# Kernel tuning notes

Measured on AMD Instinct MI355X. Metric: run time of the kernel, lower is better.

The kernel has to match this reference:

```python
import jax, jax.numpy as jnp
import numpy as np

B, T, N = 8, 512, 64        # batch, seq_len, enc_in
E, H, P = 128, 256, 96      # embed_size, hidden_size, pred_len
LAMBDA = 0.001              # softshrink sparsity threshold
SCALE = 0.02


def _leaky(h):
    return jnp.where(h >= 0, h, 0.01 * h)


def _softshrink(y):
    return jnp.where(y > LAMBDA, y - LAMBDA, jnp.where(y < -LAMBDA, y + LAMBDA, jnp.zeros_like(y)))


def setup_inputs() -> dict:
    key = jax.random.key(0)
    ks = jax.random.split(key, 16)
    f32 = jnp.float32
    d = {
        "x": jax.random.normal(ks[0], (B, T, N), f32),
        "emb": jax.random.normal(ks[1], (1, E), f32),
        # MLP (embed_size -> hidden -> embed_size), stored as [in, out]
        "w1": SCALE * jax.random.normal(ks[2], (E, H), f32),
        "b1": SCALE * jax.random.normal(ks[3], (H,), f32),
        "w2": SCALE * jax.random.normal(ks[4], (H, E), f32),
        "b2": SCALE * jax.random.normal(ks[5], (E,), f32),
        # MLP_time (seq_len -> hidden -> seq_len)
        "tw1": SCALE * jax.random.normal(ks[6], (T, H), f32),
        "tb1": SCALE * jax.random.normal(ks[7], (H,), f32),
        "tw2": SCALE * jax.random.normal(ks[8], (H, T), f32),
        "tb2": SCALE * jax.random.normal(ks[9], (T,), f32),
        # fc (seq_len*embed -> hidden -> pred_len)
        "fw1": SCALE * jax.random.normal(ks[10], (T * E, H), f32),
        "fb1": SCALE * jax.random.normal(ks[11], (H,), f32),
        "fw2": SCALE * jax.random.normal(ks[12], (H, P), f32),
        "fb2": SCALE * jax.random.normal(ks[13], (P,), f32),
    }
    return d


def reference(x, emb, w1, b1, w2, b2, tw1, tb1, tw2, tb2, fw1, fb1, fw2, fb2):
    # x: [B, T, N]
    x_noD = jnp.transpose(x, (0, 2, 1))            # [B, N, T]
    xe = x_noD[..., None] * emb                    # tokenEmb -> [B, N, T, E]
    bias = xe + x_noD[..., None]

    # NorMLP_temporal: rfft over time, shared MLP on real/imag, softshrink, irfft
    xf = jnp.fft.rfft(xe, axis=2, norm="ortho")   # [B, N, T//2+1, E] complex64

    def mlp(z):
        return _leaky(z @ w1 + b1) @ w2 + b2

    yr = _softshrink(mlp(xf.real))
    yi = _softshrink(mlp(xf.imag))
    y = jax.lax.complex(yr, yi)
    xt = jnp.fft.irfft(y, n=T, axis=2, norm="ortho")  # [B, N, T, E]

    # NorMLP_temporal_WO_freq: MLP_time over last (time) dim of x_noD
    xn = _leaky(x_noD @ tw1 + tb1) @ tw2 + tb2        # [B, N, T]

    out = xt + xn[..., None] + bias                   # use_bias = 1

    flat = out.reshape(B, N, T * E)
    h = _leaky(flat @ fw1 + fb1) @ fw2 + fb2          # [B, N, P]
    return jnp.transpose(h, (0, 2, 1))                # [B, P, N]
```

## Files before the change

kernel.cpp:

```cpp
#include <hip/hip_runtime.h>
#include <hip/hip_bf16.h>


typedef unsigned int uint;
typedef unsigned short ushort_t;
typedef __attribute__((ext_vector_type(4))) float f32x4;
typedef __attribute__((ext_vector_type(8))) short short8;

#define LAMBDA_ 0.001f
#define RSQRT512 0.044194173824159220f

__device__ __forceinline__ ushort_t f2bf(float f) {
    uint u = __float_as_uint(f);
    uint r = (u + 0x7FFFu + ((u >> 16) & 1u)) >> 16;
    return (ushort_t)r;
}
__device__ __forceinline__ ushort_t f2bf_hw(float f) {
    union { __hip_bfloat16 h; ushort_t u; } c;
    c.h = __float2bfloat16(f);
    return c.u;
}
__device__ __forceinline__ float bf2f(ushort_t v) { return __uint_as_float(((uint)v) << 16); }
__device__ __forceinline__ float leaky_(float v) { return v >= 0.f ? v : 0.01f * v; }

__device__ __forceinline__ void gload_lds16(const ushort_t* g, ushort_t* l) {
    __builtin_amdgcn_global_load_lds((const __attribute__((address_space(1))) void*)g,
                                     (__attribute__((address_space(3))) void*)l, 16, 0, 0);
}

__device__ __forceinline__ void tile_loop512(const ushort_t* __restrict__ A, int lda,
                                             const ushort_t* __restrict__ Bm, int ldb,
                                             int m0, int n0, int k0, int kIters,
                                             f32x4 (&acc)[4][2],
                                             ushort_t (&As)[2][128 * 64], ushort_t (&Bs)[2][128 * 64],
                                             int tid, int lane, int wid, int wr, int wc) {
    int lrow = lane >> 3;
    int sg = (lane & 7) ^ lrow;
    auto issue = [&](int kt, int buf) {
        int kb = k0 + kt * 64;
        for (int i = 0; i < 2; ++i) {
            int rbase = wid * 16 + i * 8;
            gload_lds16(A + (size_t)(m0 + rbase + lrow) * lda + kb + sg * 8, &As[buf][wid * 1024 + i * 512]);
            gload_lds16(Bm + (size_t)(n0 + rbase + lrow) * ldb + kb + sg * 8, &Bs[buf][wid * 1024 + i * 512]);
        }
    };
    issue(0, 0);
    __syncthreads();
    int cur = 0;
    for (int kt = 0; kt < kIters; ++kt) {
        int nxt = cur ^ 1;
        if (kt + 1 < kIters) issue(kt + 1, nxt);
        __builtin_amdgcn_s_setprio(1);
        for (int ks = 0; ks < 2; ++ks) {
            short8 a[4], b[2];
            int sl = ks * 4 + (lane >> 4);
            for (int mi = 0; mi < 4; ++mi) {
                int row = wr * 64 + mi * 16 + (lane & 15);
                a[mi] = *(const short8*)&As[cur][row * 64 + ((sl ^ (row & 7)) << 3)];
            }
            for (int ni = 0; ni < 2; ++ni) {
                int row = wc * 32 + ni * 16 + (lane & 15);
                b[ni] = *(const short8*)&Bs[cur][row * 64 + ((sl ^ (row & 7)) << 3)];
            }
            for (int mi = 0; mi < 4; ++mi)
                for (int ni = 0; ni < 2; ++ni)
                    acc[mi][ni] = __builtin_amdgcn_mfma_f32_16x16x32_bf16(a[mi], b[ni], acc[mi][ni], 0, 0, 0);
        }
        __builtin_amdgcn_s_setprio(0);
        __syncthreads();
        cur = nxt;
    }
}

__global__ __launch_bounds__(256) void k_pre_plus(const float* __restrict__ x, const float* __restrict__ tw1,
                                                  const float* __restrict__ tw2, const float* __restrict__ fw1,
                                                  const float* __restrict__ emb, const float* __restrict__ w1,
                                                  const float* __restrict__ b1,
                                                  ushort_t* __restrict__ A1cat, ushort_t* __restrict__ B1cat,
                                                  ushort_t* __restrict__ Wt, ushort_t* __restrict__ tw2_bf,
                                                  ushort_t* __restrict__ fw1T,
                                                  float* __restrict__ u_g, int* __restrict__ idxs_g,
                                                  float* __restrict__ bpkey_g) {
    __shared__ float tile[64 * 65];
    __shared__ float key_s[256];
    __shared__ int idx_s[256];
    int bid = blockIdx.x;
    int tid = threadIdx.x;
    if (bid < 3072) {
        int region = bid >> 10;
        int id = ((bid & 1023) << 8) + tid;
        int a = id >> 9, c = id & 511;
        if (region == 0) {
            int f = (a <= 256) ? a : (a - 256);
            int m = (c * f) & 511;
            float ang = (float)m * (6.283185307179586f / 512.0f);
            float v = ((a <= 256) ? cosf(ang) : -sinf(ang)) * RSQRT512;
            ushort_t hi = f2bf(v);
            ushort_t lo = f2bf(v - bf2f(hi));
            size_t row = (size_t)a * 1536;
            B1cat[row + c] = hi;
            B1cat[row + 512 + c] = hi;
            B1cat[row + 1024 + c] = lo;
        } else if (region == 1) {
            int f = (a <= 256) ? a : (a - 256);
            int m = (c * f) & 511;
            float ang = (float)m * (6.283185307179586f / 512.0f);
            float v = ((a <= 256) ? cosf(ang) : -sinf(ang)) * RSQRT512;
            float sc = (a == 0 || a == 256) ? 1.0f : 2.0f;
            Wt[id] = f2bf(v * sc);
        } else {
            if ((bid & 1023) < 512) tw2_bf[id] = f2bf(tw2[id]);
        }
    } else if (bid < 3104) {
        int b = bid - 3072;
        int t0 = (b & 7) << 6, h0 = (b >> 3) << 6;
        float (*t64)[65] = (float(*)[65])tile;
        for (int i = 0; i < 16; ++i) {
            int idx = tid + i * 256;
            int r = idx >> 6, cc = idx & 63;
            t64[r][cc] = tw1[(size_t)(t0 + r) * 256 + h0 + cc];
        }
        __syncthreads();
        for (int i = 0; i < 16; ++i) {
            int idx = tid + i * 256;
            int rr = idx >> 6, cc2 = idx & 63;
            float v = t64[cc2][rr];
            ushort_t hi = f2bf(v);
            ushort_t lo = f2bf(v - bf2f(hi));
            size_t row = (size_t)(512 + h0 + rr) * 1536;
            int t = t0 + cc2;
            B1cat[row + t] = hi;
            B1cat[row + 512 + t] = hi;
            B1cat[row + 1024 + t] = lo;
        }
    } else if (bid < 3360) {
        int b = bid - 3104;
        int bb = b >> 5;
        int rem = b & 31;
        int t0 = (rem >> 1) << 5;
        int n0 = (rem & 1) << 5;
        int tx = tid & 31, ty = tid >> 5;
        float (*t32)[33] = (float(*)[33])tile;
        for (int i = 0; i < 4; ++i) {
            int tt = ty * 4 + i;
            t32[tt][tx] = x[(size_t)(bb * 512 + t0 + tt) * 64 + n0 + tx];
        }
        __syncthreads();
        for (int i = 0; i < 4; ++i) {
            int nn = ty * 4 + i;
            float v = t32[tx][nn];
            ushort_t hi = f2bf(v);
            ushort_t lo = f2bf(v - bf2f(hi));
            size_t row = (size_t)(bb * 64 + n0 + nn) * 1536;
            int t = t0 + tx;
            A1cat[row + t] = hi;
            A1cat[row + 512 + t] = lo;
            A1cat[row + 1024 + t] = hi;
        }
    } else if (bid < 7456) {
        int b = bid - 3360;
        int e  = b & 127;
        int hb = (b >> 7) & 3;
        int tt = b >> 9;
        int t0 = tt << 6, h0 = hb << 6;
        float (*t64)[65] = (float(*)[65])tile;
        for (int i = 0; i < 4; ++i) {
            int idx = tid + i * 256;
            int r = idx >> 4, c4 = idx & 15;
            const float* src = fw1 + ((size_t)(t0 + r) * 128 + e) * 256 + h0 + c4 * 4;
            float4 v = *(const float4*)src;
            t64[r][c4 * 4 + 0] = v.x;
            t64[r][c4 * 4 + 1] = v.y;
            t64[r][c4 * 4 + 2] = v.z;
            t64[r][c4 * 4 + 3] = v.w;
        }
        __syncthreads();
        for (int p = 0; p < 2; ++p) {
            int idx = tid + p * 256;
            int hh = idx >> 3, tg = idx & 7;
            short8 o;
            for (int j = 0; j < 8; ++j) o[j] = (short)f2bf(t64[tg * 8 + j][hh]);
            *(short8*)(fw1T + ((size_t)(h0 + hh) * 128 + e) * 512 + t0 + tg * 8) = o;
        }
    } else {
        float acc = 0.f;
#pragma unroll 8
        for (int e = 0; e < 128; ++e) acc += emb[e] * w1[e * 256 + tid];
        u_g[tid] = acc;
        float bb0 = b1[tid];
        key_s[tid] = (acc == 0.f) ? INFINITY : (-bb0 / acc);
        idx_s[tid] = tid;
        __syncthreads();
        for (int k = 2; k <= 256; k <<= 1) {
            for (int j = k >> 1; j > 0; j >>= 1) {
                int ixj = tid ^ j;
                if (ixj > tid) {
                    bool up = ((tid & k) == 0);
                    float a0 = key_s[tid], a1 = key_s[ixj];
                    if ((a0 > a1) == up) {
                        key_s[tid] = a1; key_s[ixj] = a0;
                        int t0 = idx_s[tid]; idx_s[tid] = idx_s[ixj]; idx_s[ixj] = t0;
                    }
                }
                __syncthreads();
            }
        }
        bpkey_g[tid] = key_s[tid];
        idxs_g[tid] = idx_s[tid];
    }
}

__global__ __launch_bounds__(256) void k_mid(const ushort_t* __restrict__ fw1T, const float* __restrict__ emb,
                                             const float* __restrict__ tb2,
                                             ushort_t* __restrict__ B1cat, ushort_t* __restrict__ F1sbf,
                                             float* __restrict__ p2v,
                                             const float* __restrict__ u_g, const float* __restrict__ b1,
                                             const float* __restrict__ w2, const float* __restrict__ b2,
                                             const int* __restrict__ idxs_g,
                                             ushort_t* __restrict__ Atab, ushort_t* __restrict__ Btab) {
    __shared__ float embs[128];
    __shared__ float red[256];
    __shared__ float sA[256], sB[256];
    int bid = blockIdx.x;
    int tid = threadIdx.x;
    if (bid < 256) {
        int h = bid;
        if (tid < 128) embs[tid] = 1.f + emb[tid];
        __syncthreads();
        int t2 = tid * 2;
        const ushort_t* base = fw1T + ((size_t)h << 16) + t2;
        float as0 = 0.f, as1 = 0.f, ae0 = 0.f, ae1 = 0.f;
#pragma unroll 4
        for (int e = 0; e < 128; ++e) {
            uint v = *(const uint*)(base + (size_t)e * 512);
            float v0 = bf2f((ushort_t)(v & 0xffff));
            float v1 = bf2f((ushort_t)(v >> 16));
            float w = embs[e];
            as0 += v0; as1 += v1;
            ae0 += w * v0; ae1 += w * v1;
        }
        *(uint*)(F1sbf + (size_t)h * 512 + t2) = (uint)f2bf(as0) | ((uint)f2bf(as1) << 16);
        ushort_t hi0 = f2bf(ae0), hi1 = f2bf(ae1);
        ushort_t lo0 = f2bf(ae0 - bf2f(hi0)), lo1 = f2bf(ae1 - bf2f(hi1));
        size_t row = (size_t)(768 + h) * 1536;
        uint hpk = (uint)hi0 | ((uint)hi1 << 16);
        *(uint*)(B1cat + row + t2) = hpk;
        *(uint*)(B1cat + row + 512 + t2) = hpk;
        *(uint*)(B1cat + row + 1024 + t2) = (uint)lo0 | ((uint)lo1 << 16);
        red[tid] = tb2[t2] * as0 + tb2[t2 + 1] * as1;
        __syncthreads();
        for (int off = 128; off > 0; off >>= 1) {
            if (tid < off) red[tid] += red[tid + off];
            __syncthreads();
        }
        if (tid == 0) p2v[h] = red[0];
    } else {
        int e = bid - 256, r = tid;
        float uu0 = u_g[r], bb0 = b1[r];
        float w0 = w2[r * 128 + e];
        float c = (uu0 < 0.f || (uu0 == 0.f && bb0 >= 0.f)) ? 1.0f : 0.01f;
        float bA = c * uu0 * w0, bB = c * bb0 * w0;
        int h = idxs_g[r];
        float uu = u_g[h], bb = b1[h];
        float w = w2[h * 128 + e];
        float sgn = (uu > 0.f) ? 0.99f : -0.99f;
        float dA = sgn * uu * w, dB = sgn * bb * w;
        sA[r] = bA; sB[r] = bB;
        __syncthreads();
        for (int off = 128; off > 0; off >>= 1) {
            if (r < off) { sA[r] += sA[r + off]; sB[r] += sB[r + off]; }
            __syncthreads();
        }
        float baseA = sA[0], baseB = sB[0] + b2[e];
        __syncthreads();
        sA[r] = dA; sB[r] = dB;
        __syncthreads();
        for (int off = 1; off < 256; off <<= 1) {
            float vA = (r >= off) ? sA[r - off] : 0.f;
            float vB = (r >= off) ? sB[r - off] : 0.f;
            __syncthreads();
            sA[r] += vA; sB[r] += vB;
            __syncthreads();
        }
        if (r == 0) { Atab[e] = f2bf(baseA); Btab[e] = f2bf(baseB); }
        Atab[(r + 1) * 128 + e] = f2bf(baseA + sA[r]);
        Btab[(r + 1) * 128 + e] = f2bf(baseB + sB[r]);
    }
}

__global__ __launch_bounds__(512) void k_big3(const ushort_t* __restrict__ Wt, const ushort_t* __restrict__ fw1T,
                                              ushort_t* __restrict__ M2T,
                                              const ushort_t* __restrict__ A1cat, const ushort_t* __restrict__ B1cat,
                                              float* __restrict__ partialG,
                                              const ushort_t* __restrict__ tw2bf, const ushort_t* __restrict__ F1sbf,
                                              ushort_t* __restrict__ P2T) {
    __shared__ ushort_t As[2][128 * 64];
    __shared__ ushort_t Bs[2][128 * 64];
    int tid = threadIdx.x;
    int lane = tid & 63, wid = tid >> 6;
    int wr = wid >> 2, wc = wid & 3;
    int bid = blockIdx.x;
    f32x4 acc[4][2] = {};
    if (bid < 1024) {
        int xx = bid & 7, y = bid >> 3;
        int mt = y & 3;
        int nt = ((y >> 2) << 3) | xx;
        int m0 = mt * 128, n0 = nt * 128;
        tile_loop512(Wt, 512, fw1T, 512, m0, n0, 0, 8, acc, As, Bs, tid, lane, wid, wr, wc);
        ushort_t* cstage = &As[0][0];
        for (int mi = 0; mi < 4; ++mi) {
            int ml = wr * 64 + mi * 16 + ((lane >> 4) << 2);
            for (int ni = 0; ni < 2; ++ni) {
                int nl = wc * 32 + ni * 16 + (lane & 15);
                for (int r = 0; r < 4; ++r) {
                    int row = ml + r;
                    cstage[row * 128 + (nl ^ ((row & 7) << 4))] = f2bf(acc[mi][ni][r]);
                }
            }
        }
        __syncthreads();
        short8* d8 = (short8*)(M2T + ((size_t)(n0 >> 7) << 16) + (size_t)m0 * 128);
        for (int i = 0; i < 4; ++i) {
            int p = tid + i * 512;
            int row = p >> 4;
            int col0 = (p & 15) * 8;
            d8[p] = *(const short8*)&cstage[row * 128 + (col0 ^ ((row & 7) << 4))];
        }
    } else if (bid < 1280) {
        int b = bid - 1024;
        int kch = b & 7, tilei = b >> 3;
        int nt = tilei & 7, mt = tilei >> 3;
        int m0 = mt * 128, n0 = nt * 128;
        tile_loop512(A1cat, 1536, B1cat, 1536, m0, n0, kch * 192, 3, acc, As, Bs, tid, lane, wid, wr, wc);
        float* pbase = partialG + (size_t)kch * 524288;
        int mb0 = m0 + wr * 64 + ((lane >> 4) << 2);
        int nb0 = n0 + wc * 32 + (lane & 15);
        for (int mi = 0; mi < 4; ++mi)
            for (int ni = 0; ni < 2; ++ni) {
                int mbase = mb0 + mi * 16;
                int n = nb0 + ni * 16;
                for (int r = 0; r < 4; ++r)
                    pbase[(size_t)(mbase + r) * 1024 + n] = acc[mi][ni][r];
            }
    } else {
        int b = bid - 1280;
        int nt = b & 1, mt = b >> 1;
        int m0 = mt * 128, n0 = nt * 128;
        tile_loop512(tw2bf, 512, F1sbf, 512, m0, n0, 0, 8, acc, As, Bs, tid, lane, wid, wr, wc);
        int mb0 = m0 + wr * 64 + ((lane >> 4) << 2);
        int nb0 = n0 + wc * 32 + (lane & 15);
        for (int mi = 0; mi < 4; ++mi)
            for (int ni = 0; ni < 2; ++ni) {
                int mbase = mb0 + mi * 16;
                int n = nb0 + ni * 16;
                ushort4 o;
                o.x = f2bf(acc[mi][ni][0]);
                o.y = f2bf(acc[mi][ni][1]);
                o.z = f2bf(acc[mi][ni][2]);
                o.w = f2bf(acc[mi][ni][3]);
                *(ushort4*)(P2T + (size_t)n * 256 + mbase) = o;
            }
    }
}

__global__ __launch_bounds__(512) void k_gemm1(const float* __restrict__ partialG,
                                               const ushort_t* __restrict__ Atab, const ushort_t* __restrict__ Btab,
                                               const float* __restrict__ bpkey,
                                               const ushort_t* __restrict__ Bm,
                                               float* __restrict__ partial) {
    __shared__ ushort_t As[2][128 * 64];
    __shared__ ushort_t Bs[2][256 * 64];
    __shared__ float sv_s[1024];
    __shared__ ushort_t r_s[1024];
    __shared__ float bp_s[256];
    int tid = threadIdx.x;
    int lane = tid & 63, wid = tid >> 6;
    int wr = wid >> 2, wc = wid & 3;
    int bid = blockIdx.x;
    int xcd = bid & 7, j = bid >> 3;
    int kcl = j & 7, mt = j >> 3;
    int kc = xcd * 8 + kcl;
    int m0 = mt * 128;
    int k0 = kc * 1024;
    if (tid < 256) bp_s[tid] = bpkey[tid];
    __syncthreads();
    {
        int row = tid >> 2, j2 = (tid & 3) * 2;
        const float* pg = partialG + (size_t)(m0 + row) * 1024 + kc * 8 + j2;
        for (int q = 0; q < 2; ++q) {
            float sv = 0.f;
#pragma unroll
            for (int kch = 0; kch < 8; ++kch)
                sv += pg[(size_t)kch * 524288 + q];
            int lo = 0, hi = 256;
            while (lo < hi) { int mid = (lo + hi) >> 1; if (bp_s[mid] <= sv) lo = mid + 1; else hi = mid; }
            sv_s[row * 8 + j2 + q] = sv;
            r_s[row * 8 + j2 + q] = (ushort_t)lo;
        }
    }
    __syncthreads();

    int lrow = lane >> 3;
    int sg = (lane & 7) ^ lrow;
    auto issueB = [&](int kt, int buf) {
        int kb = k0 + kt * 64;
        for (int i = 0; i < 4; ++i) {
            int rbase = wid * 32 + i * 8;
            gload_lds16(Bm + (size_t)(rbase + lrow) * 65536 + kb + sg * 8, &Bs[buf][wid * 2048 + i * 512]);
        }
    };
    short8 ta[2], tb[2];
    float svr[2];
    auto gather = [&](int kt) {
        int kl = kt >> 1;
        for (int i = 0; i < 2; ++i) {
            int q = tid + i * 512;
            int row = q >> 3, slot = q & 7;
            int e0 = ((kt & 1) << 6) + slot * 8;
            int r = r_s[row * 8 + kl];
            svr[i] = sv_s[row * 8 + kl];
            ta[i] = *(const short8*)(Atab + r * 128 + e0);
            tb[i] = *(const short8*)(Btab + r * 128 + e0);
        }
    };
    auto cookwrite = [&](int buf) {
        for (int i = 0; i < 2; ++i) {
            int q = tid + i * 512;
            int row = q >> 3, slot = q & 7;
            float sv = svr[i];
            short8 o;
            for (int jj = 0; jj < 8; ++jj) {
                float y = fmaf(sv, bf2f((ushort_t)ta[i][jj]), bf2f((ushort_t)tb[i][jj]));
                y = y - fminf(fmaxf(y, -LAMBDA_), LAMBDA_);
                o[jj] = (short)f2bf_hw(y);
            }
            *(short8*)&As[buf][row * 64 + ((slot ^ (row & 7)) << 3)] = o;
        }
    };

    f32x4 acc[4][4] = {};
    issueB(0, 0);
    gather(0);
    cookwrite(0);
    __syncthreads();
    int cur = 0;
    for (int kt = 0; kt < 16; ++kt) {
        int nxt = cur ^ 1;
        if (kt + 1 < 16) { issueB(kt + 1, nxt); gather(kt + 1); }
        __builtin_amdgcn_s_setprio(1);
        for (int ks = 0; ks < 2; ++ks) {
            short8 a[4], b[4];
            int sl = ks * 4 + (lane >> 4);
            for (int mi = 0; mi < 4; ++mi) {
                int row = wr * 64 + mi * 16 + (lane & 15);
                a[mi] = *(const short8*)&As[cur][row * 64 + ((sl ^ (row & 7)) << 3)];
            }
            for (int ni = 0; ni < 4; ++ni) {
                int row = wc * 64 + ni * 16 + (lane & 15);
                b[ni] = *(const short8*)&Bs[cur][row * 64 + ((sl ^ (row & 7)) << 3)];
            }
            for (int mi = 0; mi < 4; ++mi)
                for (int ni = 0; ni < 4; ++ni)
                    acc[mi][ni] = __builtin_amdgcn_mfma_f32_16x16x32_bf16(a[mi], b[ni], acc[mi][ni], 0, 0, 0);
        }
        __builtin_amdgcn_s_setprio(0);
        if (kt + 1 < 16) cookwrite(nxt);
        __syncthreads();
        cur = nxt;
    }
    int mb0 = m0 + wr * 64 + ((lane >> 4) << 2);
    int nb0 = wc * 64 + (lane & 15);
    float* pbase = partial + (size_t)kc * 131072;
    for (int mi = 0; mi < 4; ++mi)
        for (int ni = 0; ni < 4; ++ni) {
            int mbase = mb0 + mi * 16;
            int n = nb0 + ni * 16;
            for (int r = 0; r < 4; ++r)
                pbase[(size_t)(mbase + r) * 256 + n] = acc[mi][ni][r];
        }
}

__global__ __launch_bounds__(128) void k_final(const float* __restrict__ partial, const float* __restrict__ partialG,
                                               const ushort_t* __restrict__ P2T, const float* __restrict__ p2v,
                                               const float* __restrict__ tb1, const float* __restrict__ fb1,
                                               const float* __restrict__ fw2, const float* __restrict__ fb2,
                                               float* __restrict__ out) {
    __shared__ float a_s[256];
    __shared__ float hl_s[256];
    __shared__ float hc_s[256];
    int bn = blockIdx.x;
    int tid = threadIdx.x;
    for (int q = 0; q < 2; ++q) {
        int i = tid * 2 + q;
        float a1 = 0.f, a2 = 0.f;
#pragma unroll
        for (int kch = 0; kch < 8; ++kch) {
            const float* pg = partialG + (size_t)kch * 524288 + (size_t)bn * 1024;
            a1 += pg[512 + i];
            a2 += pg[768 + i];
        }
        hl_s[i] = leaky_(a1 + tb1[i]);
        hc_s[i] = a2;
    }
    __syncthreads();
    for (int p = 0; p < 2; ++p) {
        int i = tid + p * 128;
        float acc = p2v[i] + hc_s[i] + fb1[i];
#pragma unroll 8
        for (int kc = 0; kc < 64; ++kc)
            acc += partial[((size_t)kc * 512 + bn) * 256 + i];
        const ushort_t* prow = P2T + (size_t)i * 256;
#pragma unroll 4
        for (int jb = 0; jb < 32; ++jb) {
            short8 pv = *(const short8*)(prow + jb * 8);
            for (int j8 = 0; j8 < 8; ++j8)
                acc += hl_s[jb * 8 + j8] * bf2f((ushort_t)pv[j8]);
        }
        a_s[i] = leaky_(acc);
    }
    __syncthreads();
    if (tid < 96) {
        float acc = fb2[tid];
        for (int hh = 0; hh < 256; ++hh)
            acc += a_s[hh] * fw2[hh * 96 + tid];
        int b = bn >> 6, n = bn & 63;
        out[(size_t)(b * 96 + tid) * 64 + n] = acc;
    }
}

extern "C" void kernel_launch(void* const* d_in, const int* in_sizes, int n_in,
                              void* d_out, int out_size, void* d_ws, size_t ws_size,
                              hipStream_t stream) {
    const float* x   = (const float*)d_in[0];
    const float* emb = (const float*)d_in[1];
    const float* w1  = (const float*)d_in[2];
    const float* b1  = (const float*)d_in[3];
    const float* w2  = (const float*)d_in[4];
    const float* b2  = (const float*)d_in[5];
    const float* tw1 = (const float*)d_in[6];
    const float* tb1 = (const float*)d_in[7];
    const float* tw2 = (const float*)d_in[8];
    const float* tb2 = (const float*)d_in[9];
    const float* fw1 = (const float*)d_in[10];
    const float* fb1 = (const float*)d_in[11];
    const float* fw2 = (const float*)d_in[12];
    const float* fb2 = (const float*)d_in[13];
    float* out = (float*)d_out;

    char* W = (char*)d_ws;
    size_t off = 0;
    auto take = [&](size_t bytes) { size_t r = off; off += (bytes + 255) & ~(size_t)255; return r; };
    ushort_t* fw1T  = (ushort_t*)(W + take(33554432));
    ushort_t* M2T   = (ushort_t*)(W + take(33554432));
    float* partial  = (float*)(W + take(64 * 512 * 256 * 4));
    float* partialG = (float*)(W + take(8 * 512 * 1024 * 4));
    ushort_t* A1cat = (ushort_t*)(W + take(512 * 1536 * 2));
    ushort_t* B1cat = (ushort_t*)(W + take(1024 * 1536 * 2));
    ushort_t* Wt    = (ushort_t*)(W + take(512 * 512 * 2));
    ushort_t* tw2bf = (ushort_t*)(W + take(256 * 512 * 2));
    ushort_t* F1sbf = (ushort_t*)(W + take(256 * 512 * 2));
    ushort_t* P2T   = (ushort_t*)(W + take(256 * 256 * 2));
    float* p2v      = (float*)(W + take(256 * 4));
    ushort_t* Atab  = (ushort_t*)(W + take(257 * 128 * 2));
    ushort_t* Btab  = (ushort_t*)(W + take(257 * 128 * 2));
    float* bpkey    = (float*)(W + take(256 * 4));
    float* u_g      = (float*)(W + take(256 * 4));
    int* idxs_g     = (int*)(W + take(256 * 4));
    (void)ws_size; (void)in_sizes; (void)n_in; (void)out_size;

    k_pre_plus<<<7457, 256, 0, stream>>>(x, tw1, tw2, fw1, emb, w1, b1,
                                         A1cat, B1cat, Wt, tw2bf, fw1T, u_g, idxs_g, bpkey);
    k_mid<<<384, 256, 0, stream>>>(fw1T, emb, tb2, B1cat, F1sbf, p2v,
                                   u_g, b1, w2, b2, idxs_g, Atab, Btab);
    k_big3<<<1284, 512, 0, stream>>>(Wt, fw1T, M2T, A1cat, B1cat, partialG, tw2bf, F1sbf, P2T);
    k_gemm1<<<256, 512, 0, stream>>>(partialG, Atab, Btab, bpkey, M2T, partial);
    k_final<<<512, 128, 0, stream>>>(partial, partialG, P2T, p2v, tb1, fb1, fw2, fb2, out);
}
```

Measured before the change: 137.4 us.

## Triple-buffer gemm1 prefetch and store split-K partials as bf16 via LDS staging

```diff
diff --git a/kernel.cpp b/kernel.cpp
--- a/kernel.cpp
+++ b/kernel.cpp
@@ -367,9 +367,9 @@
                                                const ushort_t* __restrict__ Atab, const ushort_t* __restrict__ Btab,
                                                const float* __restrict__ bpkey,
                                                const ushort_t* __restrict__ Bm,
-                                               float* __restrict__ partial) {
-    __shared__ ushort_t As[2][128 * 64];
-    __shared__ ushort_t Bs[2][256 * 64];
+                                               ushort_t* __restrict__ partial) {
+    __shared__ ushort_t As[3][128 * 64];
+    __shared__ ushort_t Bs[3][256 * 64];
     __shared__ float sv_s[1024];
     __shared__ ushort_t r_s[1024];
     __shared__ float bp_s[256];
@@ -439,48 +439,64 @@
     };
 
     f32x4 acc[4][4] = {};
-    issueB(0, 0);
-    gather(0);
+    gather(0); issueB(0, 0);
+    asm volatile("s_waitcnt vmcnt(4)" ::: "memory");
     cookwrite(0);
-    __syncthreads();
-    int cur = 0;
+    gather(1); issueB(1, 1);
+    asm volatile("s_waitcnt vmcnt(4)" ::: "memory");
+    cookwrite(1);
+    asm volatile("s_waitcnt lgkmcnt(0)" ::: "memory");
+    __builtin_amdgcn_s_barrier();
+    __builtin_amdgcn_sched_barrier(0);
+
     for (int kt = 0; kt < 16; ++kt) {
-        int nxt = cur ^ 1;
-        if (kt + 1 < 16) { issueB(kt + 1, nxt); gather(kt + 1); }
+        int c = kt % 3;
+        if (kt + 2 < 16) { gather(kt + 2); issueB(kt + 2, (kt + 2) % 3); }
         __builtin_amdgcn_s_setprio(1);
         for (int ks = 0; ks < 2; ++ks) {
             short8 a[4], b[4];
             int sl = ks * 4 + (lane >> 4);
             for (int mi = 0; mi < 4; ++mi) {
                 int row = wr * 64 + mi * 16 + (lane & 15);
-                a[mi] = *(const short8*)&As[cur][row * 64 + ((sl ^ (row & 7)) << 3)];
+                a[mi] = *(const short8*)&As[c][row * 64 + ((sl ^ (row & 7)) << 3)];
             }
             for (int ni = 0; ni < 4; ++ni) {
                 int row = wc * 64 + ni * 16 + (lane & 15);
-                b[ni] = *(const short8*)&Bs[cur][row * 64 + ((sl ^ (row & 7)) << 3)];
+                b[ni] = *(const short8*)&Bs[c][row * 64 + ((sl ^ (row & 7)) << 3)];
             }
             for (int mi = 0; mi < 4; ++mi)
                 for (int ni = 0; ni < 4; ++ni)
                     acc[mi][ni] = __builtin_amdgcn_mfma_f32_16x16x32_bf16(a[mi], b[ni], acc[mi][ni], 0, 0, 0);
         }
         __builtin_amdgcn_s_setprio(0);
-        if (kt + 1 < 16) cookwrite(nxt);
-        __syncthreads();
-        cur = nxt;
-    }
-    int mb0 = m0 + wr * 64 + ((lane >> 4) << 2);
+        if (kt + 2 < 16) {
+            asm volatile("s_waitcnt vmcnt(4)" ::: "memory");
+            cookwrite((kt + 2) % 3);
+        } else {
+            asm volatile("s_waitcnt vmcnt(0)" ::: "memory");
+        }
+        asm volatile("s_waitcnt lgkmcnt(0)" ::: "memory");
+        __builtin_amdgcn_s_barrier();
+        __builtin_amdgcn_sched_barrier(0);
+    }
+
+    ushort_t* cstage = &Bs[0][0];
+    int mb0l = wr * 64 + ((lane >> 4) << 2);
     int nb0 = wc * 64 + (lane & 15);
-    float* pbase = partial + (size_t)kc * 131072;
     for (int mi = 0; mi < 4; ++mi)
         for (int ni = 0; ni < 4; ++ni) {
-            int mbase = mb0 + mi * 16;
+            int rowb = mb0l + mi * 16;
             int n = nb0 + ni * 16;
             for (int r = 0; r < 4; ++r)
-                pbase[(size_t)(mbase + r) * 256 + n] = acc[mi][ni][r];
-        }
-}
-
-__global__ __launch_bounds__(128) void k_final(const float* __restrict__ partial, const float* __restrict__ partialG,
+                cstage[(rowb + r) * 256 + n] = f2bf_hw(acc[mi][ni][r]);
+        }
+    __syncthreads();
+    short8* d8 = (short8*)(partial + (size_t)kc * 131072 + (size_t)m0 * 256);
+    const short8* s8 = (const short8*)cstage;
+    for (int i = 0; i < 8; ++i) d8[tid + i * 512] = s8[tid + i * 512];
+}
+
+__global__ __launch_bounds__(128) void k_final(const ushort_t* __restrict__ partial, const float* __restrict__ partialG,
                                                const ushort_t* __restrict__ P2T, const float* __restrict__ p2v,
                                                const float* __restrict__ tb1, const float* __restrict__ fb1,
                                                const float* __restrict__ fw2, const float* __restrict__ fb2,
@@ -508,7 +524,7 @@
         float acc = p2v[i] + hc_s[i] + fb1[i];
 #pragma unroll 8
         for (int kc = 0; kc < 64; ++kc)
-            acc += partial[((size_t)kc * 512 + bn) * 256 + i];
+            acc += bf2f(partial[((size_t)kc * 512 + bn) * 256 + i]);
         const ushort_t* prow = P2T + (size_t)i * 256;
 #pragma unroll 4
         for (int jb = 0; jb < 32; ++jb) {
@@ -550,22 +566,22 @@
     char* W = (char*)d_ws;
     size_t off = 0;
     auto take = [&](size_t bytes) { size_t r = off; off += (bytes + 255) & ~(size_t)255; return r; };
-    ushort_t* fw1T  = (ushort_t*)(W + take(33554432));
-    ushort_t* M2T   = (ushort_t*)(W + take(33554432));
-    float* partial  = (float*)(W + take(64 * 512 * 256 * 4));
-    float* partialG = (float*)(W + take(8 * 512 * 1024 * 4));
-    ushort_t* A1cat = (ushort_t*)(W + take(512 * 1536 * 2));
-    ushort_t* B1cat = (ushort_t*)(W + take(1024 * 1536 * 2));
-    ushort_t* Wt    = (ushort_t*)(W + take(512 * 512 * 2));
-    ushort_t* tw2bf = (ushort_t*)(W + take(256 * 512 * 2));
-    ushort_t* F1sbf = (ushort_t*)(W + take(256 * 512 * 2));
-    ushort_t* P2T   = (ushort_t*)(W + take(256 * 256 * 2));
-    float* p2v      = (float*)(W + take(256 * 4));
-    ushort_t* Atab  = (ushort_t*)(W + take(257 * 128 * 2));
-    ushort_t* Btab  = (ushort_t*)(W + take(257 * 128 * 2));
-    float* bpkey    = (float*)(W + take(256 * 4));
-    float* u_g      = (float*)(W + take(256 * 4));
-    int* idxs_g     = (int*)(W + take(256 * 4));
+    ushort_t* fw1T   = (ushort_t*)(W + take(33554432));
+    ushort_t* M2T    = (ushort_t*)(W + take(33554432));
+    ushort_t* partial= (ushort_t*)(W + take(64 * 512 * 256 * 2));
+    float* partialG  = (float*)(W + take(8 * 512 * 1024 * 4));
+    ushort_t* A1cat  = (ushort_t*)(W + take(512 * 1536 * 2));
+    ushort_t* B1cat  = (ushort_t*)(W + take(1024 * 1536 * 2));
+    ushort_t* Wt     = (ushort_t*)(W + take(512 * 512 * 2));
+    ushort_t* tw2bf  = (ushort_t*)(W + take(256 * 512 * 2));
+    ushort_t* F1sbf  = (ushort_t*)(W + take(256 * 512 * 2));
+    ushort_t* P2T    = (ushort_t*)(W + take(256 * 256 * 2));
+    float* p2v       = (float*)(W + take(256 * 4));
+    ushort_t* Atab   = (ushort_t*)(W + take(257 * 128 * 2));
+    ushort_t* Btab   = (ushort_t*)(W + take(257 * 128 * 2));
+    float* bpkey     = (float*)(W + take(256 * 4));
+    float* u_g       = (float*)(W + take(256 * 4));
+    int* idxs_g      = (int*)(W + take(256 * 4));
     (void)ws_size; (void)in_sizes; (void)n_in; (void)out_size;
 
     k_pre_plus<<<7457, 256, 0, stream>>>(x, tw1, tw2, fw1, emb, w1, b1,
```

After: 136.3 us. Within noise of the previous version (-0.8%).
